# Kernel tuning notes

Hardware: AMD Instinct MI355X
Metric: run time of the kernel (lower is better)

The kernel has to match this reference:

```python
import jax, jax.numpy as jnp
import numpy as np

LAYER_BS = 63
N_SITES = 12
B = 2048


def _kaiming_uniform(key, shape, fan_in):
    # torch kaiming_uniform_ with a=0: bound = sqrt(6/fan_in)
    bound = np.sqrt(6.0 / fan_in)
    return jax.random.uniform(key, shape, jnp.float32, -bound, bound)


def _cnn12(x, w):
    # x: (B, L, 12, Cin); w: (L, 3*Cin, Cout)
    nn0 = jnp.roll(x, -1, axis=-2) + jnp.roll(x, 3, axis=-2)
    nnn0 = jnp.roll(x, -2, axis=-2) + jnp.roll(x, 4, axis=-2)
    c0 = jnp.concatenate([nn0, nnn0], axis=-1)          # (B,L,12,2*Cin)
    c1 = c0 + jnp.roll(c0, -2, axis=-2)
    allc = jnp.concatenate([x, c1], axis=-1)            # (B,L,12,3*Cin)
    return jnp.einsum('blsc,lco->blso', allc, w)


def _batch_linear(x, w, b):
    # x: (B, L, F); w: (L, F, O); b: (L, O)
    return jnp.einsum('blf,lfo->blo', x, w) + b


def setup_inputs() -> dict:
    key = jax.random.key(0)
    ks = jax.random.split(key, 9)
    zs = jax.random.normal(ks[0], (B, LAYER_BS, N_SITES, 2), jnp.float32)
    # CNN weights: (L, 3*Cin, Cout); kaiming fan_in = 3*Cin
    w1 = _kaiming_uniform(ks[1], (LAYER_BS, 6, 32), 6)
    w2 = _kaiming_uniform(ks[2], (LAYER_BS, 96, 64), 96)
    fw1 = _kaiming_uniform(ks[3], (LAYER_BS, 128, 64), 128)
    fb1 = jax.random.uniform(ks[4], (LAYER_BS, 64), jnp.float32, -1 / np.sqrt(128), 1 / np.sqrt(128))
    fw2 = _kaiming_uniform(ks[5], (LAYER_BS, 64, 64), 64)
    fb2 = jax.random.uniform(ks[6], (LAYER_BS, 64), jnp.float32, -1 / np.sqrt(64), 1 / np.sqrt(64))
    fw3 = _kaiming_uniform(ks[7], (LAYER_BS, 64, 1), 64)
    fb3 = jax.random.uniform(ks[8], (LAYER_BS, 1), jnp.float32, -1 / np.sqrt(64), 1 / np.sqrt(64))
    return {"zs": zs, "w1": w1, "w2": w2, "fw1": fw1, "fb1": fb1,
            "fw2": fw2, "fb2": fb2, "fw3": fw3, "fb3": fb3}


def reference(zs, w1, w2, fw1, fb1, fw2, fb2, fw3, fb3):
    h = jax.nn.relu(_cnn12(zs, w1))                     # (B,L,12,32)
    h = jax.nn.relu(_cnn12(h, w2))                      # (B,L,12,64)
    h = jnp.concatenate([h.mean(axis=-2), h.max(axis=-2)], axis=-1)
    h = jax.nn.relu(_batch_linear(h, fw1, fb1))
    h = jax.nn.relu(_batch_linear(h, fw2, fb2))
    out = _batch_linear(h, fw3, fb3)                    # (B,L,1)
    return out[..., 0]                                  # (B,L)
```

## Files before the change

kernel.cpp:

```cpp
#include <hip/hip_runtime.h>


#define LNUM 63
#define BT 16
#define NBT 128
#define WSL 19968

typedef __attribute__((ext_vector_type(8))) _Float16 half8;
typedef __attribute__((ext_vector_type(2))) _Float16 half2v;
typedef __attribute__((ext_vector_type(4))) float floatx4;
typedef __attribute__((ext_vector_type(4))) unsigned uint4v;

static __device__ __forceinline__ unsigned cvtpk(float a, float b) {
    return __builtin_bit_cast(unsigned, __builtin_amdgcn_cvt_pkrtz(a, b));
}
static __device__ __forceinline__ half2v u2h(unsigned u) { return __builtin_bit_cast(half2v, u); }
static __device__ __forceinline__ float hlo16(unsigned short s) {
    return (float)__builtin_bit_cast(_Float16, s);
}
static __device__ __forceinline__ int w12(int v) { return v >= 12 ? v - 12 : v; }
static __device__ __forceinline__ float2 add2(float2 a, float2 b) { return make_float2(a.x + b.x, a.y + b.y); }

#define O_W2DW   4160
#define O_POOLDW 3072
#define O_POOLUS 6144
#define O_POOL2  0
#define O_G2     1280

__global__ void prep(const float* __restrict__ w2, const float* __restrict__ fw1,
                     const float* __restrict__ fw2, unsigned short* __restrict__ ws) {
    __shared__ float S[8192];
    const int l = blockIdx.x, r = blockIdx.y, t = threadIdx.x;
    if (r == 0) {
        const float4* src = (const float4*)(w2 + (size_t)l * 6144);
        #pragma unroll
        for (int j = 0; j < 6; ++j) *(float4*)(S + 4 * (t + 256 * j)) = src[t + 256 * j];
        __syncthreads();
        unsigned* dst = (unsigned*)(ws + (size_t)l * WSL);
        #pragma unroll
        for (int j = 0; j < 13; ++j) {
            int i = j * 256 + t, o = i / 52, cp = i - 52 * o, c = 2 * cp;
            dst[i] = cvtpk(S[c * 64 + o], S[c * 64 + 64 + o]);
        }
    } else if (r == 1) {
        const float4* src = (const float4*)(fw1 + (size_t)l * 8192);
        #pragma unroll
        for (int j = 0; j < 8; ++j) *(float4*)(S + 4 * (t + 256 * j)) = src[t + 256 * j];
        __syncthreads();
        unsigned* dst = (unsigned*)(ws + (size_t)l * WSL + 6656);
        #pragma unroll
        for (int j = 0; j < 17; ++j) {
            int i = j * 256 + t, o = i / 68, cp = i - 68 * o;
            dst[i] = cvtpk(S[cp * 64 + o], S[(64 + cp) * 64 + o]);
        }
    } else {
        const float4* src = (const float4*)(fw2 + (size_t)l * 4096);
        #pragma unroll
        for (int j = 0; j < 4; ++j) *(float4*)(S + 4 * (t + 256 * j)) = src[t + 256 * j];
        __syncthreads();
        unsigned* dst = (unsigned*)(ws + (size_t)l * WSL + 15360);
        #pragma unroll
        for (int j = 0; j < 9; ++j) {
            int i = j * 256 + t, o = i / 36, cp = i - 36 * o, c = 2 * cp;
            dst[i] = cvtpk(S[c * 64 + o], S[c * 64 + 64 + o]);
        }
    }
}

__global__ __launch_bounds__(256, 5) void fused_nn(
    const float* __restrict__ zs,  const float* __restrict__ w1,
    const float* __restrict__ fb1, const float* __restrict__ fb2,
    const float* __restrict__ fw3, const float* __restrict__ fb3,
    const unsigned short* __restrict__ ws,
    float* __restrict__ out)
{
    __shared__ __align__(16) unsigned U[7488];
    unsigned short* USH = (unsigned short*)U;

    const int t    = threadIdx.x;
    const int lane = t & 63;
    const int wv   = t >> 6;
    const int n    = lane & 15;
    const int quad = lane >> 4;
    const int l    = blockIdx.x / NBT;
    const int b0   = (blockIdx.x % NBT) * BT;

    {
        const uint4v* src = (const uint4v*)(ws + (size_t)l * WSL);
        uint4v s0 = src[t];
        uint4v s1 = src[t + 256];
        uint4v s2 = src[t + 512];
        uint4v s3 = (t < 64) ? src[t + 768] : (uint4v){0, 0, 0, 0};
        uint4v* dst = (uint4v*)(U + O_W2DW);
        dst[t]       = s0;
        dst[t + 256] = s1;
        dst[t + 512] = s2;
        if (t < 64) dst[t + 768] = s3;
    }

    {
        const int b = t >> 4, cpair = t & 15, c0 = cpair * 2;
        const float* xb = zs + ((size_t)(b0 + b) * LNUM + l) * 24;
        float2 xv[12];
        #pragma unroll
        for (int q = 0; q < 6; ++q) {
            float4 xq = *(const float4*)(xb + q * 4);
            xv[2 * q]     = make_float2(xq.x, xq.y);
            xv[2 * q + 1] = make_float2(xq.z, xq.w);
        }
        const float* wl = w1 + (size_t)l * 192 + c0;
        const float2 w0  = *(const float2*)(wl);
        const float2 w1v = *(const float2*)(wl + 32);
        const float2 w2v = *(const float2*)(wl + 64);
        const float2 w3v = *(const float2*)(wl + 96);
        const float2 w4v = *(const float2*)(wl + 128);
        const float2 w5v = *(const float2*)(wl + 160);
        #pragma unroll
        for (int s = 0; s < 12; ++s) {
            float2 xA = add2(add2(xv[w12(s + 1)], xv[w12(s + 11)]),
                             add2(xv[w12(s + 3)], xv[w12(s + 9)]));
            float2 xB = add2(add2(xv[w12(s + 2)], xv[w12(s + 10)]),
                             add2(xv[w12(s + 4)], xv[w12(s + 8)]));
            float hx = xv[s].x*w0.x + xv[s].y*w1v.x + xA.x*w2v.x + xA.y*w3v.x
                     + xB.x*w4v.x + xB.y*w5v.x;
            float hy = xv[s].x*w0.y + xv[s].y*w1v.y + xA.x*w2v.y + xA.y*w3v.y
                     + xB.x*w4v.y + xB.y*w5v.y;
            U[(b * 12 + s) * 20 + cpair] = cvtpk(fmaxf(hx, 0.f), fmaxf(hy, 0.f));
        }
    }
    const float bias1 = fb1[(size_t)l * 64 + wv * 16 + n];
    const float bias2 = fb2[(size_t)l * 64 + wv * 16 + n];
    __syncthreads();

    floatx4 acc[3][4];
    #pragma unroll
    for (int mi = 0; mi < 3; ++mi)
        #pragma unroll
        for (int nt = 0; nt < 4; ++nt) acc[mi][nt] = (floatx4){0.f, 0.f, 0.f, 0.f};
    {
        int rbq[3], a20[3];
        #pragma unroll
        for (int mi = 0; mi < 3; ++mi) {
            int row = 48 * wv + 16 * mi + n;
            int bi = row / 12;
            int si = row - 12 * bi;
            rbq[mi] = bi * 240 + quad * 4;
            a20[mi] = si * 20;
        }
        const uint4v* w2l = (const uint4v*)(U + O_W2DW);
        const int c13 = n * 13 + quad;
        constexpr int tapd[9] = {0, 1, 11, 3, 9, 2, 10, 4, 8};
        uint4v bw[4];
        #pragma unroll
        for (int i = 0; i < 9; ++i) {
            const int sec = (i == 0) ? 0 : (i < 5 ? 1 : 2);
            if (i == 0 || i == 1 || i == 5) {
                #pragma unroll
                for (int nt = 0; nt < 4; ++nt)
                    bw[nt] = w2l[c13 + nt * 208 + sec * 4];
            }
            half8 af[3];
            #pragma unroll
            for (int mi = 0; mi < 3; ++mi) {
                int off = a20[mi] + tapd[i] * 20;
                if (tapd[i]) { if (off >= 240) off -= 240; }
                af[mi] = *(const half8*)(U + rbq[mi] + off);
            }
            #pragma unroll
            for (int mi = 0; mi < 3; ++mi)
                #pragma unroll
                for (int nt = 0; nt < 4; ++nt)
                    acc[mi][nt] = __builtin_amdgcn_mfma_f32_16x16x32_f16(
                        af[mi], __builtin_bit_cast(half8, bw[nt]), acc[mi][nt], 0, 0, 0);
        }
    }
    __syncthreads();

    #pragma unroll
    for (int mi = 0; mi < 3; ++mi) {
        const int rr = 48 * wv + 16 * mi + 4 * quad;
        const int bq = rr / 12;
        const int chk = (rr - 12 * bq) >> 2;
        #pragma unroll
        for (int nt = 0; nt < 4; ++nt) {
            const int ch = nt * 16 + n;
            float r0 = fmaxf(acc[mi][nt][0], 0.f), r1 = fmaxf(acc[mi][nt][1], 0.f);
            float r2 = fmaxf(acc[mi][nt][2], 0.f), r3 = fmaxf(acc[mi][nt][3], 0.f);
            float sm = (r0 + r1) + (r2 + r3);
            float mx = fmaxf(fmaxf(r0, r1), fmaxf(r2, r3));
            U[(bq * 64 + ch) * 3 + chk] = cvtpk(sm, mx);
        }
    }
    __builtin_amdgcn_wave_barrier();

    {
        const unsigned* p = U + t * 12;
        uint4v q0 = *(const uint4v*)(p);
        uint4v q1 = *(const uint4v*)(p + 4);
        uint4v q2 = *(const uint4v*)(p + 8);
        unsigned arr[12] = {q0.x, q0.y, q0.z, q0.w, q1.x, q1.y, q1.z, q1.w,
                            q2.x, q2.y, q2.z, q2.w};
        const int b = t >> 4, ch0 = (t * 4) & 63;
        const _Float16 inv12 = (_Float16)(1.0f / 12.0f);
        unsigned pk[4];
        #pragma unroll
        for (int j = 0; j < 4; ++j) {
            half2v d0 = u2h(arr[3 * j]), d1 = u2h(arr[3 * j + 1]), d2 = u2h(arr[3 * j + 2]);
            _Float16 s = (d0[0] + d1[0]) + d2[0];
            _Float16 m0 = d0[1] > d1[1] ? d0[1] : d1[1];
            _Float16 m  = m0 > d2[1] ? m0 : d2[1];
            half2v pm;
            pm[0] = s * inv12;
            pm[1] = m;
            pk[j] = __builtin_bit_cast(unsigned, pm);
        }
        uint2 w01 = make_uint2(pk[0], pk[1]), w23 = make_uint2(pk[2], pk[3]);
        *(uint2*)(U + O_POOLDW + b * 68 + ch0)     = w01;
        *(uint2*)(U + O_POOLDW + b * 68 + ch0 + 2) = w23;
    }
    __syncthreads();

    {
        const int o = wv * 16 + n;
        floatx4 a1 = (floatx4){bias1, bias1, bias1, bias1};
        const uint4v* f1q = (const uint4v*)(ws + (size_t)l * WSL + 6656);
        #pragma unroll
        for (int ks = 0; ks < 4; ++ks) {
            half8 av = *(const half8*)(USH + O_POOLUS + n * 136 + ks * 32 + quad * 8);
            uint4v bw = f1q[o * 17 + ks * 4 + quad];
            a1 = __builtin_amdgcn_mfma_f32_16x16x32_f16(av, __builtin_bit_cast(half8, bw), a1, 0, 0, 0);
        }
        #pragma unroll
        for (int i = 0; i < 2; ++i) {
            unsigned pk = cvtpk(fmaxf(a1[2 * i], 0.f), fmaxf(a1[2 * i + 1], 0.f));
            USH[O_POOL2 + (quad * 4 + 2 * i)     * 72 + o] = (unsigned short)(pk & 0xffffu);
            USH[O_POOL2 + (quad * 4 + 2 * i + 1) * 72 + o] = (unsigned short)(pk >> 16);
        }
    }
    __syncthreads();

    {
        const int o = wv * 16 + n;
        floatx4 a2 = (floatx4){bias2, bias2, bias2, bias2};
        const uint4v* f2q = (const uint4v*)(ws + (size_t)l * WSL + 15360);
        #pragma unroll
        for (int ks = 0; ks < 2; ++ks) {
            half8 av = *(const half8*)(USH + O_POOL2 + n * 72 + ks * 32 + quad * 8);
            uint4v bw = f2q[o * 9 + ks * 4 + quad];
            a2 = __builtin_amdgcn_mfma_f32_16x16x32_f16(av, __builtin_bit_cast(half8, bw), a2, 0, 0, 0);
        }
        #pragma unroll
        for (int i = 0; i < 2; ++i) {
            unsigned pk = cvtpk(fmaxf(a2[2 * i], 0.f), fmaxf(a2[2 * i + 1], 0.f));
            USH[O_G2 + (quad * 4 + 2 * i)     * 72 + o] = (unsigned short)(pk & 0xffffu);
            USH[O_G2 + (quad * 4 + 2 * i + 1) * 72 + o] = (unsigned short)(pk >> 16);
        }
    }
    __syncthreads();

    if (t < 16) {
        float a = fb3[l];
        const float* w3 = fw3 + (size_t)l * 64;
        #pragma unroll
        for (int c4 = 0; c4 < 16; ++c4) {
            uint2 u2 = *(const uint2*)(USH + O_G2 + t * 72 + c4 * 4);
            float4 w = *(const float4*)(w3 + c4 * 4);
            a += hlo16((unsigned short)(u2.x & 0xffff)) * w.x
               + hlo16((unsigned short)(u2.x >> 16))    * w.y
               + hlo16((unsigned short)(u2.y & 0xffff)) * w.z
               + hlo16((unsigned short)(u2.y >> 16))    * w.w;
        }
        out[(size_t)(b0 + t) * LNUM + l] = a;
    }
}

extern "C" void kernel_launch(void* const* d_in, const int* in_sizes, int n_in,
                              void* d_out, int out_size, void* d_ws, size_t ws_size,
                              hipStream_t stream) {
    const float* zs  = (const float*)d_in[0];
    const float* w1  = (const float*)d_in[1];
    const float* w2  = (const float*)d_in[2];
    const float* fw1 = (const float*)d_in[3];
    const float* fb1 = (const float*)d_in[4];
    const float* fw2 = (const float*)d_in[5];
    const float* fb2 = (const float*)d_in[6];
    const float* fw3 = (const float*)d_in[7];
    const float* fb3 = (const float*)d_in[8];
    float* out = (float*)d_out;
    unsigned short* ws = (unsigned short*)d_ws;

    hipLaunchKernelGGL(prep, dim3(LNUM, 3), dim3(256), 0, stream, w2, fw1, fw2, ws);
    hipLaunchKernelGGL(fused_nn, dim3(LNUM * NBT), dim3(256), 0, stream,
                       zs, w1, fb1, fb2, fw3, fb3, ws, out);
}
```

Before: 146.6 us.

## Double batch tile per block and pre-sum CNN taps before MFMA

Each block now handles 32 batch rows with 512 threads instead of 16 with 256. This amortizes the per-layer w2 weight staging into LDS over twice the work and halves the block count. The second conv now sums the four neighbour-tap fp16 A fragments before the MFMA, cutting the K steps from 9 to 3 per tile. That moves adds into fp16 vector ops, which can lose some precision, and it raises LDS use per block, which may lower occupancy.

```diff
diff --git a/kernel.cpp b/kernel.cpp
--- a/kernel.cpp
+++ b/kernel.cpp
@@ -2,8 +2,8 @@
 
 
 #define LNUM 63
-#define BT 16
-#define NBT 128
+#define BT 32
+#define NBT 64
 #define WSL 19968
 
 typedef __attribute__((ext_vector_type(8))) _Float16 half8;
@@ -21,11 +21,11 @@
 static __device__ __forceinline__ int w12(int v) { return v >= 12 ? v - 12 : v; }
 static __device__ __forceinline__ float2 add2(float2 a, float2 b) { return make_float2(a.x + b.x, a.y + b.y); }
 
-#define O_W2DW   4160
-#define O_POOLDW 3072
-#define O_POOLUS 6144
+#define O_W2DW   7680
+#define O_POOLDW 7680
+#define O_POOLUS 15360
 #define O_POOL2  0
-#define O_G2     1280
+#define O_G2     2304
 
 __global__ void prep(const float* __restrict__ w2, const float* __restrict__ fw1,
                      const float* __restrict__ fw2, unsigned short* __restrict__ ws) {
@@ -67,14 +67,14 @@
     }
 }
 
-__global__ __launch_bounds__(256, 5) void fused_nn(
+__global__ __launch_bounds__(512, 4) void fused_nn(
     const float* __restrict__ zs,  const float* __restrict__ w1,
     const float* __restrict__ fb1, const float* __restrict__ fb2,
     const float* __restrict__ fw3, const float* __restrict__ fb3,
     const unsigned short* __restrict__ ws,
     float* __restrict__ out)
 {
-    __shared__ __align__(16) unsigned U[7488];
+    __shared__ __align__(16) unsigned U[11008];
     unsigned short* USH = (unsigned short*)U;
 
     const int t    = threadIdx.x;
@@ -87,15 +87,15 @@
 
     {
         const uint4v* src = (const uint4v*)(ws + (size_t)l * WSL);
+        uint4v* dst = (uint4v*)(U + O_W2DW);
         uint4v s0 = src[t];
-        uint4v s1 = src[t + 256];
-        uint4v s2 = src[t + 512];
-        uint4v s3 = (t < 64) ? src[t + 768] : (uint4v){0, 0, 0, 0};
-        uint4v* dst = (uint4v*)(U + O_W2DW);
-        dst[t]       = s0;
-        dst[t + 256] = s1;
-        dst[t + 512] = s2;
-        if (t < 64) dst[t + 768] = s3;
+        if (t < 320) {
+            uint4v s1 = src[512 + t];
+            dst[t] = s0;
+            dst[512 + t] = s1;
+        } else {
+            dst[t] = s0;
+        }
     }
 
     {
@@ -128,8 +128,10 @@
             U[(b * 12 + s) * 20 + cpair] = cvtpk(fmaxf(hx, 0.f), fmaxf(hy, 0.f));
         }
     }
-    const float bias1 = fb1[(size_t)l * 64 + wv * 16 + n];
-    const float bias2 = fb2[(size_t)l * 64 + wv * 16 + n];
+    const int mt = wv >> 2;
+    const int oc = (wv & 3) * 16 + n;
+    const float bias1 = fb1[(size_t)l * 64 + oc];
+    const float bias2 = fb2[(size_t)l * 64 + oc];
     __syncthreads();
 
     floatx4 acc[3][4];
@@ -138,33 +140,38 @@
         #pragma unroll
         for (int nt = 0; nt < 4; ++nt) acc[mi][nt] = (floatx4){0.f, 0.f, 0.f, 0.f};
     {
-        int rbq[3], a20[3];
+        int rbq[3], si_[3];
         #pragma unroll
         for (int mi = 0; mi < 3; ++mi) {
-            int row = 48 * wv + 16 * mi + n;
-            int bi = row / 12;
-            int si = row - 12 * bi;
+            int rowm = 16 * mi + n;
+            int bi = 4 * wv + rowm / 12;
+            si_[mi] = rowm % 12;
             rbq[mi] = bi * 240 + quad * 4;
-            a20[mi] = si * 20;
         }
         const uint4v* w2l = (const uint4v*)(U + O_W2DW);
         const int c13 = n * 13 + quad;
-        constexpr int tapd[9] = {0, 1, 11, 3, 9, 2, 10, 4, 8};
-        uint4v bw[4];
-        #pragma unroll
-        for (int i = 0; i < 9; ++i) {
-            const int sec = (i == 0) ? 0 : (i < 5 ? 1 : 2);
-            if (i == 0 || i == 1 || i == 5) {
-                #pragma unroll
-                for (int nt = 0; nt < 4; ++nt)
-                    bw[nt] = w2l[c13 + nt * 208 + sec * 4];
-            }
+        const int dA[4] = {1, 11, 3, 9};
+        const int dB[4] = {2, 10, 4, 8};
+        #pragma unroll
+        for (int ks = 0; ks < 3; ++ks) {
+            uint4v bw[4];
+            #pragma unroll
+            for (int nt = 0; nt < 4; ++nt)
+                bw[nt] = w2l[c13 + nt * 208 + ks * 4];
             half8 af[3];
             #pragma unroll
             for (int mi = 0; mi < 3; ++mi) {
-                int off = a20[mi] + tapd[i] * 20;
-                if (tapd[i]) { if (off >= 240) off -= 240; }
-                af[mi] = *(const half8*)(U + rbq[mi] + off);
+                const int s = si_[mi], base = rbq[mi];
+                if (ks == 0) {
+                    af[mi] = *(const half8*)(U + base + s * 20);
+                } else {
+                    const int* d = (ks == 1) ? dA : dB;
+                    half8 l0 = *(const half8*)(U + base + w12(s + d[0]) * 20);
+                    half8 l1 = *(const half8*)(U + base + w12(s + d[1]) * 20);
+                    half8 l2 = *(const half8*)(U + base + w12(s + d[2]) * 20);
+                    half8 l3 = *(const half8*)(U + base + w12(s + d[3]) * 20);
+                    af[mi] = (l0 + l1) + (l2 + l3);
+                }
             }
             #pragma unroll
             for (int mi = 0; mi < 3; ++mi)
@@ -221,44 +228,42 @@
     __syncthreads();
 
     {
-        const int o = wv * 16 + n;
         floatx4 a1 = (floatx4){bias1, bias1, bias1, bias1};
         const uint4v* f1q = (const uint4v*)(ws + (size_t)l * WSL + 6656);
         #pragma unroll
         for (int ks = 0; ks < 4; ++ks) {
-            half8 av = *(const half8*)(USH + O_POOLUS + n * 136 + ks * 32 + quad * 8);
-            uint4v bw = f1q[o * 17 + ks * 4 + quad];
+            half8 av = *(const half8*)(USH + O_POOLUS + (mt * 16 + n) * 136 + ks * 32 + quad * 8);
+            uint4v bw = f1q[oc * 17 + ks * 4 + quad];
             a1 = __builtin_amdgcn_mfma_f32_16x16x32_f16(av, __builtin_bit_cast(half8, bw), a1, 0, 0, 0);
         }
         #pragma unroll
         for (int i = 0; i < 2; ++i) {
             unsigned pk = cvtpk(fmaxf(a1[2 * i], 0.f), fmaxf(a1[2 * i + 1], 0.f));
-            USH[O_POOL2 + (quad * 4 + 2 * i)     * 72 + o] = (unsigned short)(pk & 0xffffu);
-            USH[O_POOL2 + (quad * 4 + 2 * i + 1) * 72 + o] = (unsigned short)(pk >> 16);
-        }
-    }
-    __syncthreads();
-
-    {
-        const int o = wv * 16 + n;
+            USH[O_POOL2 + (mt * 16 + quad * 4 + 2 * i)     * 72 + oc] = (unsigned short)(pk & 0xffffu);
+            USH[O_POOL2 + (mt * 16 + quad * 4 + 2 * i + 1) * 72 + oc] = (unsigned short)(pk >> 16);
+        }
+    }
+    __syncthreads();
+
+    {
         floatx4 a2 = (floatx4){bias2, bias2, bias2, bias2};
         const uint4v* f2q = (const uint4v*)(ws + (size_t)l * WSL + 15360);
         #pragma unroll
         for (int ks = 0; ks < 2; ++ks) {
-            half8 av = *(const half8*)(USH + O_POOL2 + n * 72 + ks * 32 + quad * 8);
-            uint4v bw = f2q[o * 9 + ks * 4 + quad];
+            half8 av = *(const half8*)(USH + O_POOL2 + (mt * 16 + n) * 72 + ks * 32 + quad * 8);
+            uint4v bw = f2q[oc * 9 + ks * 4 + quad];
             a2 = __builtin_amdgcn_mfma_f32_16x16x32_f16(av, __builtin_bit_cast(half8, bw), a2, 0, 0, 0);
         }
         #pragma unroll
         for (int i = 0; i < 2; ++i) {
             unsigned pk = cvtpk(fmaxf(a2[2 * i], 0.f), fmaxf(a2[2 * i + 1], 0.f));
-            USH[O_G2 + (quad * 4 + 2 * i)     * 72 + o] = (unsigned short)(pk & 0xffffu);
-            USH[O_G2 + (quad * 4 + 2 * i + 1) * 72 + o] = (unsigned short)(pk >> 16);
-        }
-    }
-    __syncthreads();
-
-    if (t < 16) {
+            USH[O_G2 + (mt * 16 + quad * 4 + 2 * i)     * 72 + oc] = (unsigned short)(pk & 0xffffu);
+            USH[O_G2 + (mt * 16 + quad * 4 + 2 * i + 1) * 72 + oc] = (unsigned short)(pk >> 16);
+        }
+    }
+    __syncthreads();
+
+    if (t < 32) {
         float a = fb3[l];
         const float* w3 = fw3 + (size_t)l * 64;
         #pragma unroll
@@ -290,6 +295,6 @@
     unsigned short* ws = (unsigned short*)d_ws;
 
     hipLaunchKernelGGL(prep, dim3(LNUM, 3), dim3(256), 0, stream, w2, fw1, fw2, ws);
-    hipLaunchKernelGGL(fused_nn, dim3(LNUM * NBT), dim3(256), 0, stream,
+    hipLaunchKernelGGL(fused_nn, dim3(LNUM * NBT), dim3(512), 0, stream,
                        zs, w1, fb1, fb2, fw3, fb3, ws, out);
 }
```

New measurement: 139.0 us. 5.2% less time.
